# Performance work log

Hardware: AMD Instinct MI355X
Metric: run time of the kernel (lower is better)

## Reference

```python
import jax, jax.numpy as jnp
import numpy as np

INPUT_SIZE = 128
HID = 64
B, T = 256, 1024

def setup_inputs() -> dict:
    key = jax.random.key(0)
    ks = jax.random.split(key, 12)
    s1 = 1.0 / np.sqrt(HID)
    def u(k, shape):
        return jax.random.uniform(k, shape, jnp.float32, -s1, s1)
    return {
        "x": jax.random.normal(ks[0], (B, T, INPUT_SIZE), jnp.float32),
        "w_ih0": u(ks[1], (4 * HID, INPUT_SIZE)),
        "w_hh0": u(ks[2], (4 * HID, HID)),
        "b_ih0": u(ks[3], (4 * HID,)),
        "b_hh0": u(ks[4], (4 * HID,)),
        "w_ih1": u(ks[5], (4 * HID, HID)),
        "w_hh1": u(ks[6], (4 * HID, HID)),
        "b_ih1": u(ks[7], (4 * HID,)),
        "b_hh1": u(ks[8], (4 * HID,)),
        "w_out": u(ks[9], (1, HID)),
        "b_out": u(ks[10], (1,)),
    }

def _lstm(x, w_ih, w_hh, b_ih, b_hh):
    # x: [B, T, I] -> h sequence [B, T, H]; PyTorch gate order i, f, g, o
    Bb = x.shape[0]
    H = w_hh.shape[1]
    # precompute input contribution for all timesteps (one big GEMM)
    xg = jnp.einsum('bti,gi->btg', x, w_ih) + b_ih + b_hh  # [B, T, 4H]
    def step(carry, g_t):
        h, c = carry
        g = g_t + h @ w_hh.T  # [B, 4H]
        i, f, gg, o = jnp.split(g, 4, axis=-1)
        i = jax.nn.sigmoid(i)
        f = jax.nn.sigmoid(f)
        gg = jnp.tanh(gg)
        o = jax.nn.sigmoid(o)
        c = f * c + i * gg
        h = o * jnp.tanh(c)
        return (h, c), h
    init = (jnp.zeros((Bb, H), x.dtype), jnp.zeros((Bb, H), x.dtype))
    _, hs = jax.lax.scan(step, init, jnp.swapaxes(xg, 0, 1))  # [T, B, H]
    return jnp.swapaxes(hs, 0, 1)

def reference(x, w_ih0, w_hh0, b_ih0, b_hh0, w_ih1, w_hh1, b_ih1, b_hh1, w_out, b_out):
    h1 = _lstm(x, w_ih0, w_hh0, b_ih0, b_hh0)   # [B, T, H]
    h2 = _lstm(h1, w_ih1, w_hh1, b_ih1, b_hh1)  # [B, T, H]
    logits = jnp.einsum('bth,oh->bto', h2, w_out) + b_out  # [B, T, 1]
    return jax.nn.sigmoid(logits)
```

## Files before the change

kernel.cpp:

```cpp
#include <hip/hip_runtime.h>

#define BB 256
#define TT 1024
#define II 128
#define HH 64
#define BT (BB * TT)

typedef _Float16 h2 __attribute__((ext_vector_type(2)));
typedef _Float16 half8 __attribute__((ext_vector_type(8)));
typedef float f32x4 __attribute__((ext_vector_type(4)));
typedef unsigned int uint;
typedef unsigned short ushort;

#define BC(u) __builtin_bit_cast(h2, (uint)(u))
#define MFMA16(a, b, c) __builtin_amdgcn_mfma_f32_16x16x32_f16((a), (b), (c), 0, 0, 0)
#define SIG(v) __builtin_amdgcn_rcpf(1.0f + __expf(-(v)))
#define TNH(v) (1.0f - 2.0f * __builtin_amdgcn_rcpf(1.0f + __expf(2.0f * (v))))

#define BAR() asm volatile("s_waitcnt lgkmcnt(0)\n\ts_barrier" ::: "memory")

__device__ __forceinline__ uint pk2(float a, float b) {
    h2 h; h[0] = (_Float16)a; h[1] = (_Float16)b;
    return __builtin_bit_cast(uint, h);
}

__global__ __launch_bounds__(256)
void xg_mfma(const float* __restrict__ x, const float* __restrict__ w_ih0,
             ushort* __restrict__ xg)
{
    __shared__ __align__(16) _Float16 xt[64][136];
    __shared__ __align__(16) _Float16 wt[128][136];
    __shared__ __align__(16) ushort   sg[64][140];
    const int tid = threadIdx.x, lane = tid & 63, wv = tid >> 6;
    const int bt0 = blockIdx.x * 64;
    const int b = bt0 >> 10, t0 = bt0 & 1023;
    {
        const int row = tid >> 2, q = (tid & 3) * 32;
        const float4* src = (const float4*)(x + (size_t)(bt0 + row) * II + q);
        _Float16* dst = &xt[row][q];
        #pragma unroll
        for (int i = 0; i < 8; ++i) {
            float4 v = src[i];
            dst[4*i+0]=(_Float16)v.x; dst[4*i+1]=(_Float16)v.y;
            dst[4*i+2]=(_Float16)v.z; dst[4*i+3]=(_Float16)v.w;
        }
    }
    for (int nh = 0; nh < 2; ++nh) {
        __syncthreads();
        {
            const int n = tid >> 1, kh = (tid & 1) * 64;
            const int flatn = nh * 128 + n;
            const int srcrow = (flatn & 3) * 64 + (flatn >> 2);
            const float4* src = (const float4*)(w_ih0 + (size_t)srcrow * II + kh);
            _Float16* dst = &wt[n][kh];
            #pragma unroll
            for (int i = 0; i < 16; ++i) {
                float4 v = src[i];
                dst[4*i+0]=(_Float16)v.x; dst[4*i+1]=(_Float16)v.y;
                dst[4*i+2]=(_Float16)v.z; dst[4*i+3]=(_Float16)v.w;
            }
        }
        __syncthreads();
        const int m = wv * 16 + (lane & 15);
        const int kf = (lane >> 4) * 8;
        half8 a0 = *(const half8*)&xt[m][ 0 + kf];
        half8 a1 = *(const half8*)&xt[m][32 + kf];
        half8 a2 = *(const half8*)&xt[m][64 + kf];
        half8 a3 = *(const half8*)&xt[m][96 + kf];
        #pragma unroll
        for (int nt = 0; nt < 8; ++nt) {
            const int nloc = nt * 16 + (lane & 15);
            half8 b0 = *(const half8*)&wt[nloc][ 0 + kf];
            half8 b1 = *(const half8*)&wt[nloc][32 + kf];
            half8 b2 = *(const half8*)&wt[nloc][64 + kf];
            half8 b3 = *(const half8*)&wt[nloc][96 + kf];
            f32x4 acc = {0.f, 0.f, 0.f, 0.f};
            acc = MFMA16(a0, b0, acc); acc = MFMA16(a1, b1, acc);
            acc = MFMA16(a2, b2, acc); acc = MFMA16(a3, b3, acc);
            const int cl = nt * 16 + (lane & 15);
            const int r0 = wv * 16 + (lane >> 4) * 4;
            #pragma unroll
            for (int r = 0; r < 4; ++r) {
                _Float16 hv = (_Float16)acc[r];
                sg[r0 + r][cl] = __builtin_bit_cast(ushort, hv);
            }
        }
        __syncthreads();
        {
            const int jl = tid >> 3, part = tid & 7;
            const int j = nh * 32 + jl;
            ushort* gdst = xg + (((size_t)b * 64 + j) << 12)
                              + (size_t)(t0 + part * 8) * 4;
            #pragma unroll
            for (int i = 0; i < 4; ++i) {
                uint2 lo = *(const uint2*)&sg[part * 8 + 2*i    ][jl * 4];
                uint2 hi = *(const uint2*)&sg[part * 8 + 2*i + 1][jl * 4];
                uint4 v; v.x = lo.x; v.y = lo.y; v.z = hi.x; v.w = hi.y;
                *(uint4*)(gdst + i * 8) = v;
            }
        }
    }
}

__global__ __launch_bounds__(192) __attribute__((amdgpu_waves_per_eu(1, 1)))
void lstm2_core(const float* __restrict__ w_hh0,
                const float* __restrict__ b_ih0, const float* __restrict__ b_hh0,
                const float* __restrict__ w_ih1, const float* __restrict__ w_hh1,
                const float* __restrict__ b_ih1, const float* __restrict__ b_hh1,
                const ushort* __restrict__ xg, ushort* __restrict__ h1g)
{
    const int bb = blockIdx.x;
    const int w  = threadIdx.x >> 6;
    const int j  = threadIdx.x & 63;
    const int qq = j >> 4, cc = j & 15;

    __shared__ __align__(16) uint  h0buf[8][32];
    __shared__ __align__(16) uint  h1buf[32];
    __shared__ __align__(16) float zbuf[8][64][4];

    const float* Wsel = (w == 0) ? w_hh0 : (w == 1) ? w_ih1 : w_hh1;
    uint4 Bf[16][2];
    #pragma unroll
    for (int t = 0; t < 16; ++t) {
        const int row = (t & 3) * 64 + (t >> 2) * 16 + cc;
        const float* rp = Wsel + (size_t)row * 64 + qq * 8;
        #pragma unroll
        for (int kh = 0; kh < 2; ++kh) {
            const float* p = rp + kh * 32;
            uint4 v;
            v.x = pk2(p[0], p[1]); v.y = pk2(p[2], p[3]);
            v.z = pk2(p[4], p[5]); v.w = pk2(p[6], p[7]);
            Bf[t][kh] = v;
        }
    }

    float bI = 0.f, bF = 0.f, bG = 0.f, bO = 0.f;
    if (w == 0) {
        bI = b_ih0[j]       + b_hh0[j];
        bF = b_ih0[64 + j]  + b_hh0[64 + j];
        bG = b_ih0[128 + j] + b_hh0[128 + j];
        bO = b_ih0[192 + j] + b_hh0[192 + j];
    } else if (w == 2) {
        bI = b_ih1[j]       + b_hh1[j];
        bF = b_ih1[64 + j]  + b_hh1[64 + j];
        bG = b_ih1[128 + j] + b_hh1[128 + j];
        bO = b_ih1[192 + j] + b_hh1[192 + j];
    }

    float cst = 0.0f;
    const ushort* xb = xg + ((size_t)(bb * 64 + j) << 12);
    ushort* h1b = h1g + (size_t)bb * TT * 64 + j;

    const f32x4 ZR4 = {0.f, 0.f, 0.f, 0.f};
    const int qlo = qq & 1, qhi = qq >> 1;

    half8 af0 = {0,0,0,0,0,0,0,0}, af1 = {0,0,0,0,0,0,0,0};
    f32x4 zr = {0.f, 0.f, 0.f, 0.f};
    uint4 q0 = {0,0,0,0}, q1 = {0,0,0,0};
    if (w == 0) {
        q0 = *(const uint4*)(xb);
        q1 = *(const uint4*)(xb + 8);
    }

#define LDAF(SRC) { const char* hb_ = (const char*)(SRC); \
    af0 = *(const half8*)(hb_ + (qq << 4)); \
    af1 = *(const half8*)(hb_ + 64 + (qq << 4)); }

#define GEMV16(SI, SF, SG, SO) { \
    f32x4 D[16]; \
    _Pragma("unroll") \
    for (int t = 0; t < 16; ++t) { \
        f32x4 d_ = MFMA16(af0, __builtin_bit_cast(half8, Bf[t][0]), ZR4); \
        D[t] = MFMA16(af1, __builtin_bit_cast(half8, Bf[t][1]), d_); } \
    { float a_, b_; \
      a_ = qlo ? D[ 4][0] : D[ 0][0]; b_ = qlo ? D[12][0] : D[ 8][0]; SI = qhi ? b_ : a_; \
      a_ = qlo ? D[ 5][0] : D[ 1][0]; b_ = qlo ? D[13][0] : D[ 9][0]; SF = qhi ? b_ : a_; \
      a_ = qlo ? D[ 6][0] : D[ 2][0]; b_ = qlo ? D[14][0] : D[10][0]; SG = qhi ? b_ : a_; \
      a_ = qlo ? D[ 7][0] : D[ 3][0]; b_ = qlo ? D[15][0] : D[11][0]; SO = qhi ? b_ : a_; } }

#define PSTEP(KK, XLO, XHI) \
    if ((KK) < TT) { \
        float si, sf, sg, so; \
        GEMV16(si, sf, sg, so) \
        h2 xlo = BC(XLO), xhi = BC(XHI); \
        si += bI + (float)xlo[0]; sf += bF + (float)xlo[1]; \
        sg += bG + (float)xhi[0]; so += bO + (float)xhi[1]; \
        float ii = SIG(si), ff = SIG(sf), gg = TNH(sg), oo = SIG(so); \
        cst = fmaf(ff, cst, ii * gg); \
        float hval = oo * TNH(cst); \
        ((_Float16*)&h0buf[(KK) & 7][0])[j] = (_Float16)hval; \
        LDAF(&h0buf[(KK) & 7][0]) \
    }

#define Q1STEP(KK) { const int i_ = (KK); \
    if (i_ >= 3 && i_ < TT + 3) { \
        const int m_ = i_ - 3; \
        float si, sf, sg, so; \
        GEMV16(si, sf, sg, so) \
        f32x4 zv = {si, sf, sg, so}; \
        *(f32x4*)&zbuf[m_ & 7][j][0] = zv; \
    } \
    if (i_ >= 2 && i_ < TT + 2) LDAF(&h0buf[(i_ - 2) & 7][0]) }

#define Q2STEP(KK) { const int i_ = (KK); \
    if (i_ >= 6) { \
        const int m_ = i_ - 6; \
        float si, sf, sg, so; \
        GEMV16(si, sf, sg, so) \
        si += bI + zr[0]; sf += bF + zr[1]; \
        sg += bG + zr[2]; so += bO + zr[3]; \
        float ii = SIG(si), ff = SIG(sf), gg = TNH(sg), oo = SIG(so); \
        cst = fmaf(ff, cst, ii * gg); \
        float hval = oo * TNH(cst); \
        _Float16 hf = (_Float16)hval; \
        ((_Float16*)&h1buf[0])[j] = hf; \
        LDAF(&h1buf[0]) \
        h1b[(size_t)m_ * 64] = __builtin_bit_cast(ushort, hf); \
    } \
    if (i_ >= 5 && i_ < TT + 5) zr = *(const f32x4*)&zbuf[(i_ - 5) & 7][j][0]; }

    for (int k0 = 0; k0 < TT + 6; k0 += 2) {
        if (w == 0) {
            uint4 qn = q1;
            if (k0 + 4 < TT)
                qn = *(const uint4*)(xb + (size_t)(k0 + 4) * 4);
            PSTEP(k0,     q0.x, q0.y)
            PSTEP(k0 + 1, q0.z, q0.w)
            q0 = q1; q1 = qn;
        } else if (w == 1) {
            Q1STEP(k0)
            Q1STEP(k0 + 1)
        } else {
            Q2STEP(k0)
            Q2STEP(k0 + 1)
        }
        BAR();
    }
#undef PSTEP
#undef Q1STEP
#undef Q2STEP
#undef GEMV16
#undef LDAF
}

__global__ __launch_bounds__(256)
void head_gemv(const ushort* __restrict__ h1g, const float* __restrict__ w_out,
               const float* __restrict__ b_out, float* __restrict__ outp)
{
    __shared__ float wsh[64];
    const int tid = threadIdx.x;
    if (tid < 64) wsh[tid] = w_out[tid];
    __syncthreads();
    const int bt = blockIdx.x * 256 + tid;
    const uint4* hp = (const uint4*)(h1g + (size_t)bt * 64);
    float s = 0.0f;
    #pragma unroll
    for (int i = 0; i < 8; ++i) {
        uint4 v = hp[i];
        const float* wp = &wsh[8 * i];
        h2 p;
        p = BC(v.x); s = fmaf((float)p[0], wp[0], s); s = fmaf((float)p[1], wp[1], s);
        p = BC(v.y); s = fmaf((float)p[0], wp[2], s); s = fmaf((float)p[1], wp[3], s);
        p = BC(v.z); s = fmaf((float)p[0], wp[4], s); s = fmaf((float)p[1], wp[5], s);
        p = BC(v.w); s = fmaf((float)p[0], wp[6], s); s = fmaf((float)p[1], wp[7], s);
    }
    outp[bt] = __builtin_amdgcn_rcpf(1.0f + __expf(-(s + b_out[0])));
}

extern "C" void kernel_launch(void* const* d_in, const int* in_sizes, int n_in,
                              void* d_out, int out_size, void* d_ws, size_t ws_size,
                              hipStream_t stream) {
    const float* x     = (const float*)d_in[0];
    const float* w_ih0 = (const float*)d_in[1];
    const float* w_hh0 = (const float*)d_in[2];
    const float* b_ih0 = (const float*)d_in[3];
    const float* b_hh0 = (const float*)d_in[4];
    const float* w_ih1 = (const float*)d_in[5];
    const float* w_hh1 = (const float*)d_in[6];
    const float* b_ih1 = (const float*)d_in[7];
    const float* b_hh1 = (const float*)d_in[8];
    const float* w_out = (const float*)d_in[9];
    const float* b_out = (const float*)d_in[10];
    float* out = (float*)d_out;

    ushort* xg  = (ushort*)d_ws;
    ushort* h1g = (ushort*)((char*)d_ws + (size_t)BT * 256 * 2);

    hipLaunchKernelGGL(xg_mfma, dim3(BT / 64), dim3(256), 0, stream, x, w_ih0, xg);
    hipLaunchKernelGGL(lstm2_core, dim3(BB), dim3(192), 0, stream,
                       w_hh0, b_ih0, b_hh0, w_ih1, w_hh1, b_ih1, b_hh1, xg, h1g);
    hipLaunchKernelGGL(head_gemv, dim3(BT / 256), dim3(256), 0, stream,
                       h1g, w_out, b_out, out);
}
```

Before: 754.4 us.

## Add dedicated store wave for layer-2 hidden states and interleave MFMA chains

Adds a fourth wave to the recurrent kernel. It copies layer-2 hidden states from a new 8-slot LDS ring to global memory with coalesced 32-bit stores, two timesteps at a time and lagging the compute by a few steps. This takes the scattered 2-byte global store off the layer-2 recurrence wave. The GEMV is also reordered into two independent passes of 16 MFMAs so consecutive MFMAs do not depend on each other, with an opaque zero accumulator. The costs are a larger block, extra loop iterations to drain the pipeline, and more LDS.

```diff
diff --git a/kernel.cpp b/kernel.cpp
--- a/kernel.cpp
+++ b/kernel.cpp
@@ -102,7 +102,7 @@
     }
 }
 
-__global__ __launch_bounds__(192) __attribute__((amdgpu_waves_per_eu(1, 1)))
+__global__ __launch_bounds__(256) __attribute__((amdgpu_waves_per_eu(1, 1)))
 void lstm2_core(const float* __restrict__ w_hh0,
                 const float* __restrict__ b_ih0, const float* __restrict__ b_hh0,
                 const float* __restrict__ w_ih1, const float* __restrict__ w_hh1,
@@ -115,22 +115,24 @@
     const int qq = j >> 4, cc = j & 15;
 
     __shared__ __align__(16) uint  h0buf[8][32];
-    __shared__ __align__(16) uint  h1buf[32];
+    __shared__ __align__(16) uint  h1q[8][32];
     __shared__ __align__(16) float zbuf[8][64][4];
 
-    const float* Wsel = (w == 0) ? w_hh0 : (w == 1) ? w_ih1 : w_hh1;
     uint4 Bf[16][2];
-    #pragma unroll
-    for (int t = 0; t < 16; ++t) {
-        const int row = (t & 3) * 64 + (t >> 2) * 16 + cc;
-        const float* rp = Wsel + (size_t)row * 64 + qq * 8;
+    if (w < 3) {
+        const float* Wsel = (w == 0) ? w_hh0 : (w == 1) ? w_ih1 : w_hh1;
         #pragma unroll
-        for (int kh = 0; kh < 2; ++kh) {
-            const float* p = rp + kh * 32;
-            uint4 v;
-            v.x = pk2(p[0], p[1]); v.y = pk2(p[2], p[3]);
-            v.z = pk2(p[4], p[5]); v.w = pk2(p[6], p[7]);
-            Bf[t][kh] = v;
+        for (int t = 0; t < 16; ++t) {
+            const int row = (t & 3) * 64 + (t >> 2) * 16 + cc;
+            const float* rp = Wsel + (size_t)row * 64 + qq * 8;
+            #pragma unroll
+            for (int kh = 0; kh < 2; ++kh) {
+                const float* p = rp + kh * 32;
+                uint4 v;
+                v.x = pk2(p[0], p[1]); v.y = pk2(p[2], p[3]);
+                v.z = pk2(p[4], p[5]); v.w = pk2(p[6], p[7]);
+                Bf[t][kh] = v;
+            }
         }
     }
 
@@ -149,9 +151,12 @@
 
     float cst = 0.0f;
     const ushort* xb = xg + ((size_t)(bb * 64 + j) << 12);
-    ushort* h1b = h1g + (size_t)bb * TT * 64 + j;
-
-    const f32x4 ZR4 = {0.f, 0.f, 0.f, 0.f};
+    uint* h1w = (uint*)(h1g + (size_t)bb * TT * 64);
+
+    float z0 = 0.f, z1 = 0.f, z2 = 0.f, z3 = 0.f;
+    asm volatile("" : "+v"(z0), "+v"(z1), "+v"(z2), "+v"(z3));
+    const f32x4 Zq = {z0, z1, z2, z3};
+
     const int qlo = qq & 1, qhi = qq >> 1;
 
     half8 af0 = {0,0,0,0,0,0,0,0}, af1 = {0,0,0,0,0,0,0,0};
@@ -169,9 +174,11 @@
 #define GEMV16(SI, SF, SG, SO) { \
     f32x4 D[16]; \
     _Pragma("unroll") \
-    for (int t = 0; t < 16; ++t) { \
-        f32x4 d_ = MFMA16(af0, __builtin_bit_cast(half8, Bf[t][0]), ZR4); \
-        D[t] = MFMA16(af1, __builtin_bit_cast(half8, Bf[t][1]), d_); } \
+    for (int t = 0; t < 16; ++t) \
+        D[t] = MFMA16(af0, __builtin_bit_cast(half8, Bf[t][0]), Zq); \
+    _Pragma("unroll") \
+    for (int t = 0; t < 16; ++t) \
+        D[t] = MFMA16(af1, __builtin_bit_cast(half8, Bf[t][1]), D[t]); \
     { float a_, b_; \
       a_ = qlo ? D[ 4][0] : D[ 0][0]; b_ = qlo ? D[12][0] : D[ 8][0]; SI = qhi ? b_ : a_; \
       a_ = qlo ? D[ 5][0] : D[ 1][0]; b_ = qlo ? D[13][0] : D[ 9][0]; SF = qhi ? b_ : a_; \
@@ -203,7 +210,7 @@
     if (i_ >= 2 && i_ < TT + 2) LDAF(&h0buf[(i_ - 2) & 7][0]) }
 
 #define Q2STEP(KK) { const int i_ = (KK); \
-    if (i_ >= 6) { \
+    if (i_ >= 6 && i_ < TT + 6) { \
         const int m_ = i_ - 6; \
         float si, sf, sg, so; \
         GEMV16(si, sf, sg, so) \
@@ -213,13 +220,12 @@
         cst = fmaf(ff, cst, ii * gg); \
         float hval = oo * TNH(cst); \
         _Float16 hf = (_Float16)hval; \
-        ((_Float16*)&h1buf[0])[j] = hf; \
-        LDAF(&h1buf[0]) \
-        h1b[(size_t)m_ * 64] = __builtin_bit_cast(ushort, hf); \
+        ((_Float16*)&h1q[m_ & 7][0])[j] = hf; \
+        LDAF(&h1q[m_ & 7][0]) \
     } \
     if (i_ >= 5 && i_ < TT + 5) zr = *(const f32x4*)&zbuf[(i_ - 5) & 7][j][0]; }
 
-    for (int k0 = 0; k0 < TT + 6; k0 += 2) {
+    for (int k0 = 0; k0 < TT + 10; k0 += 2) {
         if (w == 0) {
             uint4 qn = q1;
             if (k0 + 4 < TT)
@@ -230,9 +236,15 @@
         } else if (w == 1) {
             Q1STEP(k0)
             Q1STEP(k0 + 1)
-        } else {
+        } else if (w == 2) {
             Q2STEP(k0)
             Q2STEP(k0 + 1)
+        } else {
+            if (k0 >= 10) {
+                const int m0 = k0 - 10;
+                const uint v = ((const uint*)h1q)[((m0 & 7) << 5) + j];
+                h1w[((size_t)m0 << 5) + j] = v;
+            }
         }
         BAR();
     }
@@ -287,7 +299,7 @@
     ushort* h1g = (ushort*)((char*)d_ws + (size_t)BT * 256 * 2);
 
     hipLaunchKernelGGL(xg_mfma, dim3(BT / 64), dim3(256), 0, stream, x, w_ih0, xg);
-    hipLaunchKernelGGL(lstm2_core, dim3(BB), dim3(192), 0, stream,
+    hipLaunchKernelGGL(lstm2_core, dim3(BB), dim3(256), 0, stream,
                        w_hh0, b_ih0, b_hh0, w_ih1, w_hh1, b_ih1, b_hh1, xg, h1g);
     hipLaunchKernelGGL(head_gemv, dim3(BT / 256), dim3(256), 0, stream,
                        h1g, w_out, b_out, out);
```

New measurement: 833.0 us. 1.1x slower.

## Split each LSTM role across four waves and barrier every timestep

Applied to the files above, without the earlier changes.

The recurrent core kernel grows from 3 waves per batch row (one per role) to 12, with each role split over 4 waves that each own 16 hidden units. Each wave now issues 8 MFMAs per step instead of 32, cutting per-step latency on the serial recurrence path. In exchange it needs a block barrier after every timestep instead of every two, more LDS traffic, and a 4-deep ring buffer in place of 8, with lanes 16-63 computing redundant results that are discarded.

```diff
diff --git a/kernel.cpp b/kernel.cpp
--- a/kernel.cpp
+++ b/kernel.cpp
@@ -102,45 +102,48 @@
     }
 }
 
-__global__ __launch_bounds__(192) __attribute__((amdgpu_waves_per_eu(1, 1)))
+__global__ __launch_bounds__(768) __attribute__((amdgpu_waves_per_eu(3, 3)))
 void lstm2_core(const float* __restrict__ w_hh0,
                 const float* __restrict__ b_ih0, const float* __restrict__ b_hh0,
                 const float* __restrict__ w_ih1, const float* __restrict__ w_hh1,
                 const float* __restrict__ b_ih1, const float* __restrict__ b_hh1,
                 const ushort* __restrict__ xg, ushort* __restrict__ h1g)
 {
-    const int bb = blockIdx.x;
-    const int w  = threadIdx.x >> 6;
-    const int j  = threadIdx.x & 63;
-    const int qq = j >> 4, cc = j & 15;
-
-    __shared__ __align__(16) uint  h0buf[8][32];
-    __shared__ __align__(16) uint  h1buf[32];
-    __shared__ __align__(16) float zbuf[8][64][4];
-
-    const float* Wsel = (w == 0) ? w_hh0 : (w == 1) ? w_ih1 : w_hh1;
-    uint4 Bf[16][2];
-    #pragma unroll
-    for (int t = 0; t < 16; ++t) {
-        const int row = (t & 3) * 64 + (t >> 2) * 16 + cc;
-        const float* rp = Wsel + (size_t)row * 64 + qq * 8;
-        #pragma unroll
-        for (int kh = 0; kh < 2; ++kh) {
-            const float* p = rp + kh * 32;
-            uint4 v;
-            v.x = pk2(p[0], p[1]); v.y = pk2(p[2], p[3]);
-            v.z = pk2(p[4], p[5]); v.w = pk2(p[6], p[7]);
-            Bf[t][kh] = v;
-        }
-    }
+    const int bb   = blockIdx.x;
+    const int tid  = threadIdx.x;
+    const int w    = tid >> 6;
+    const int role = w >> 2;
+    const int p    = w & 3;
+    const int ln   = tid & 63;
+    const int qq   = ln >> 4, cc = ln & 15;
+    const int j    = p * 16 + cc;
+    const bool wr  = (ln < 16);
+
+    __shared__ __align__(16) uint  h0buf[4][32];
+    __shared__ __align__(16) uint  h1buf[4][32];
+    __shared__ __align__(16) float zbuf[4][64][4];
+
+    const float* Wsel = (role == 0) ? w_hh0 : (role == 1) ? w_ih1 : w_hh1;
+    uint4 Bf00, Bf01, Bf10, Bf11, Bf20, Bf21, Bf30, Bf31;
+#define LDBF(G, V0, V1) { \
+    const float* rp = Wsel + (size_t)((G) * 64 + j) * 64 + qq * 8; \
+    { const float* pp = rp;       uint4 v; \
+      v.x = pk2(pp[0], pp[1]); v.y = pk2(pp[2], pp[3]); \
+      v.z = pk2(pp[4], pp[5]); v.w = pk2(pp[6], pp[7]); V0 = v; } \
+    { const float* pp = rp + 32;  uint4 v; \
+      v.x = pk2(pp[0], pp[1]); v.y = pk2(pp[2], pp[3]); \
+      v.z = pk2(pp[4], pp[5]); v.w = pk2(pp[6], pp[7]); V1 = v; } }
+    LDBF(0, Bf00, Bf01) LDBF(1, Bf10, Bf11)
+    LDBF(2, Bf20, Bf21) LDBF(3, Bf30, Bf31)
+#undef LDBF
 
     float bI = 0.f, bF = 0.f, bG = 0.f, bO = 0.f;
-    if (w == 0) {
+    if (role == 0) {
         bI = b_ih0[j]       + b_hh0[j];
         bF = b_ih0[64 + j]  + b_hh0[64 + j];
         bG = b_ih0[128 + j] + b_hh0[128 + j];
         bO = b_ih0[192 + j] + b_hh0[192 + j];
-    } else if (w == 2) {
+    } else if (role == 2) {
         bI = b_ih1[j]       + b_hh1[j];
         bF = b_ih1[64 + j]  + b_hh1[64 + j];
         bG = b_ih1[128 + j] + b_hh1[128 + j];
@@ -151,95 +154,91 @@
     const ushort* xb = xg + ((size_t)(bb * 64 + j) << 12);
     ushort* h1b = h1g + (size_t)bb * TT * 64 + j;
 
-    const f32x4 ZR4 = {0.f, 0.f, 0.f, 0.f};
-    const int qlo = qq & 1, qhi = qq >> 1;
-
-    half8 af0 = {0,0,0,0,0,0,0,0}, af1 = {0,0,0,0,0,0,0,0};
-    f32x4 zr = {0.f, 0.f, 0.f, 0.f};
+    half8 af0 = {0,0,0,0,0,0,0,0}, af1 = af0;
     uint4 q0 = {0,0,0,0}, q1 = {0,0,0,0};
-    if (w == 0) {
+    if (role == 0) {
         q0 = *(const uint4*)(xb);
         q1 = *(const uint4*)(xb + 8);
     }
+
+    if (tid < 32)                 h0buf[3][tid] = 0u;
+    else if (tid < 64)            h1buf[3][tid - 32] = 0u;
+    __syncthreads();
 
 #define LDAF(SRC) { const char* hb_ = (const char*)(SRC); \
     af0 = *(const half8*)(hb_ + (qq << 4)); \
     af1 = *(const half8*)(hb_ + 64 + (qq << 4)); }
 
-#define GEMV16(SI, SF, SG, SO) { \
-    f32x4 D[16]; \
-    _Pragma("unroll") \
-    for (int t = 0; t < 16; ++t) { \
-        f32x4 d_ = MFMA16(af0, __builtin_bit_cast(half8, Bf[t][0]), ZR4); \
-        D[t] = MFMA16(af1, __builtin_bit_cast(half8, Bf[t][1]), d_); } \
-    { float a_, b_; \
-      a_ = qlo ? D[ 4][0] : D[ 0][0]; b_ = qlo ? D[12][0] : D[ 8][0]; SI = qhi ? b_ : a_; \
-      a_ = qlo ? D[ 5][0] : D[ 1][0]; b_ = qlo ? D[13][0] : D[ 9][0]; SF = qhi ? b_ : a_; \
-      a_ = qlo ? D[ 6][0] : D[ 2][0]; b_ = qlo ? D[14][0] : D[10][0]; SG = qhi ? b_ : a_; \
-      a_ = qlo ? D[ 7][0] : D[ 3][0]; b_ = qlo ? D[15][0] : D[11][0]; SO = qhi ? b_ : a_; } }
-
-#define PSTEP(KK, XLO, XHI) \
-    if ((KK) < TT) { \
-        float si, sf, sg, so; \
-        GEMV16(si, sf, sg, so) \
-        h2 xlo = BC(XLO), xhi = BC(XHI); \
-        si += bI + (float)xlo[0]; sf += bF + (float)xlo[1]; \
-        sg += bG + (float)xhi[0]; so += bO + (float)xhi[1]; \
-        float ii = SIG(si), ff = SIG(sf), gg = TNH(sg), oo = SIG(so); \
-        cst = fmaf(ff, cst, ii * gg); \
-        float hval = oo * TNH(cst); \
-        ((_Float16*)&h0buf[(KK) & 7][0])[j] = (_Float16)hval; \
-        LDAF(&h0buf[(KK) & 7][0]) \
-    }
-
-#define Q1STEP(KK) { const int i_ = (KK); \
-    if (i_ >= 3 && i_ < TT + 3) { \
-        const int m_ = i_ - 3; \
-        float si, sf, sg, so; \
-        GEMV16(si, sf, sg, so) \
-        f32x4 zv = {si, sf, sg, so}; \
-        *(f32x4*)&zbuf[m_ & 7][j][0] = zv; \
-    } \
-    if (i_ >= 2 && i_ < TT + 2) LDAF(&h0buf[(i_ - 2) & 7][0]) }
-
-#define Q2STEP(KK) { const int i_ = (KK); \
-    if (i_ >= 6) { \
-        const int m_ = i_ - 6; \
-        float si, sf, sg, so; \
-        GEMV16(si, sf, sg, so) \
-        si += bI + zr[0]; sf += bF + zr[1]; \
-        sg += bG + zr[2]; so += bO + zr[3]; \
-        float ii = SIG(si), ff = SIG(sf), gg = TNH(sg), oo = SIG(so); \
-        cst = fmaf(ff, cst, ii * gg); \
-        float hval = oo * TNH(cst); \
-        _Float16 hf = (_Float16)hval; \
-        ((_Float16*)&h1buf[0])[j] = hf; \
-        LDAF(&h1buf[0]) \
-        h1b[(size_t)m_ * 64] = __builtin_bit_cast(ushort, hf); \
-    } \
-    if (i_ >= 5 && i_ < TT + 5) zr = *(const f32x4*)&zbuf[(i_ - 5) & 7][j][0]; }
-
-    for (int k0 = 0; k0 < TT + 6; k0 += 2) {
-        if (w == 0) {
-            uint4 qn = q1;
-            if (k0 + 4 < TT)
-                qn = *(const uint4*)(xb + (size_t)(k0 + 4) * 4);
-            PSTEP(k0,     q0.x, q0.y)
-            PSTEP(k0 + 1, q0.z, q0.w)
+#define GEMV4(SI, SF, SG, SO) { \
+    const f32x4 Z_ = {0.f, 0.f, 0.f, 0.f}; \
+    f32x4 D0 = MFMA16(af0, __builtin_bit_cast(half8, Bf00), Z_); \
+    f32x4 D1 = MFMA16(af0, __builtin_bit_cast(half8, Bf10), Z_); \
+    f32x4 D2 = MFMA16(af0, __builtin_bit_cast(half8, Bf20), Z_); \
+    f32x4 D3 = MFMA16(af0, __builtin_bit_cast(half8, Bf30), Z_); \
+    D0 = MFMA16(af1, __builtin_bit_cast(half8, Bf01), D0); \
+    D1 = MFMA16(af1, __builtin_bit_cast(half8, Bf11), D1); \
+    D2 = MFMA16(af1, __builtin_bit_cast(half8, Bf21), D2); \
+    D3 = MFMA16(af1, __builtin_bit_cast(half8, Bf31), D3); \
+    SI = D0[0]; SF = D1[0]; SG = D2[0]; SO = D3[0]; }
+
+#define PBODY(K, XLO, XHI) { \
+    LDAF(&h0buf[((K) + 3) & 3][0]) \
+    float si, sf, sg, so; \
+    GEMV4(si, sf, sg, so) \
+    h2 xlo = BC(XLO), xhi = BC(XHI); \
+    si += bI + (float)xlo[0]; sf += bF + (float)xlo[1]; \
+    sg += bG + (float)xhi[0]; so += bO + (float)xhi[1]; \
+    float ii = SIG(si), ff = SIG(sf), gg = TNH(sg), oo = SIG(so); \
+    cst = fmaf(ff, cst, ii * gg); \
+    float hval = oo * TNH(cst); \
+    if (wr) ((_Float16*)&h0buf[(K) & 3][0])[j] = (_Float16)hval; }
+
+#define Q1BODY(M) { \
+    LDAF(&h0buf[(M) & 3][0]) \
+    float si, sf, sg, so; \
+    GEMV4(si, sf, sg, so) \
+    if (wr) { f32x4 zv = {si, sf, sg, so}; \
+              *(f32x4*)&zbuf[(M) & 3][j][0] = zv; } }
+
+#define Q2BODY(M) { \
+    LDAF(&h1buf[((M) + 3) & 3][0]) \
+    const f32x4 zr = *(const f32x4*)&zbuf[(M) & 3][j][0]; \
+    float si, sf, sg, so; \
+    GEMV4(si, sf, sg, so) \
+    si += bI + zr[0]; sf += bF + zr[1]; \
+    sg += bG + zr[2]; so += bO + zr[3]; \
+    float ii = SIG(si), ff = SIG(sf), gg = TNH(sg), oo = SIG(so); \
+    cst = fmaf(ff, cst, ii * gg); \
+    float hval = oo * TNH(cst); \
+    _Float16 hf = (_Float16)hval; \
+    if (wr) { ((_Float16*)&h1buf[(M) & 3][0])[j] = hf; \
+              h1b[(size_t)(M) * 64] = __builtin_bit_cast(ushort, hf); } }
+
+    for (int k0 = 0; k0 < TT + 4; k0 += 2) {
+        uint4 qn = q1;
+        if (role == 0) {
+            if (k0 + 4 < TT) qn = *(const uint4*)(xb + (size_t)(k0 + 4) * 4);
+            if (k0 < TT) PBODY(k0, q0.x, q0.y)
+        } else if (role == 1) {
+            if (k0 >= 2 && k0 < TT + 2) Q1BODY(k0 - 2)
+        } else {
+            if (k0 >= 4) Q2BODY(k0 - 4)
+        }
+        BAR();
+        if (role == 0) {
+            if (k0 + 1 < TT) PBODY(k0 + 1, q0.z, q0.w)
             q0 = q1; q1 = qn;
-        } else if (w == 1) {
-            Q1STEP(k0)
-            Q1STEP(k0 + 1)
+        } else if (role == 1) {
+            if (k0 + 1 >= 2 && k0 + 1 < TT + 2) Q1BODY(k0 - 1)
         } else {
-            Q2STEP(k0)
-            Q2STEP(k0 + 1)
+            if (k0 + 1 >= 4) Q2BODY(k0 - 3)
         }
         BAR();
     }
-#undef PSTEP
-#undef Q1STEP
-#undef Q2STEP
-#undef GEMV16
+#undef PBODY
+#undef Q1BODY
+#undef Q2BODY
+#undef GEMV4
 #undef LDAF
 }
 
@@ -287,7 +286,7 @@
     ushort* h1g = (ushort*)((char*)d_ws + (size_t)BT * 256 * 2);
 
     hipLaunchKernelGGL(xg_mfma, dim3(BT / 64), dim3(256), 0, stream, x, w_ih0, xg);
-    hipLaunchKernelGGL(lstm2_core, dim3(BB), dim3(192), 0, stream,
+    hipLaunchKernelGGL(lstm2_core, dim3(BB), dim3(768), 0, stream,
                        w_hh0, b_ih0, b_hh0, w_ih1, w_hh1, b_ih1, b_hh1, xg, h1g);
     hipLaunchKernelGGL(head_gemv, dim3(BT / 256), dim3(256), 0, stream,
                        h1g, w_out, b_out, out);
```

Result: slower. 808.0 us (+7.1%).
